# Kernel tuning notes

Hardware: AMD Instinct MI355X
Metric: run time of the kernel (lower is better)

Reference implementation:

```python
import jax, jax.numpy as jnp
import numpy as np

ALPHA = 0.2  # LeakyReLU negative slope
NEG_BIG = -9e15

def setup_inputs() -> dict:
    key = jax.random.key(0)
    k1, k2, k3, k4 = jax.random.split(key, 4)
    N, Fin, Fout = 8192, 256, 64
    h = jax.random.normal(k1, (N, Fin), dtype=jnp.float32)
    adj = jax.random.randint(k2, (N, N), 0, 2, dtype=jnp.int32)
    W = jax.random.normal(k3, (Fin, Fout), dtype=jnp.float32) * 0.1
    a = jax.random.normal(k4, (2 * Fout, 1), dtype=jnp.float32) * 0.1
    return {"h": h, "adj": adj, "W": W, "a": a}

def reference(h, adj, W, a):
    Fout = W.shape[1]
    Wh = h @ W                                # [N, Fout]
    # e_ij = leakyrelu([Wh_i ; Wh_j] . a) = leakyrelu(Wh_i.a1 + Wh_j.a2)
    a1 = a[:Fout, 0]                          # [Fout]
    a2 = a[Fout:, 0]                          # [Fout]
    s1 = Wh @ a1                              # [N]
    s2 = Wh @ a2                              # [N]
    e = jax.nn.leaky_relu(s1[:, None] + s2[None, :], negative_slope=ALPHA)  # [N, N]
    attention = jnp.where(adj > 0, e, jnp.float32(NEG_BIG))
    attention = jax.nn.softmax(attention, axis=1)
    # dropout p=0.0 (eval) -> identity
    h_prime = attention @ Wh                  # [N, Fout]
    return jax.nn.elu(h_prime)                # concat=True
```

## Files before the change

kernel.cpp:

```cpp
#include <hip/hip_runtime.h>
#include <hip/hip_bf16.h>


typedef __attribute__((ext_vector_type(8))) short bf16x8;
typedef __attribute__((ext_vector_type(16))) float f32x16;

#define LOG2E 1.4426950408889634f

__device__ __forceinline__ uint pk2o(float a, float b) {
    __hip_bfloat162 h = __float22bfloat162_rn(make_float2(a, b));
    union { __hip_bfloat162 b; uint u; } c; c.b = h; return c.u;
}
__device__ __forceinline__ ushort f2bf(float x) {
    union { __hip_bfloat16 b; ushort u; } c;
    c.b = __float2bfloat16(x);
    return c.u;
}
__device__ __forceinline__ float bf2f(ushort u) {
    union { ushort u; __hip_bfloat16 b; } c;
    c.u = u;
    return __bfloat162float(c.b);
}

__global__ __launch_bounds__(256) void k1_wh(
    const float* __restrict__ h, const float* __restrict__ W,
    const float* __restrict__ a,
    float* __restrict__ s1, float* __restrict__ Fg, float* __restrict__ Gg,
    ushort* __restrict__ pw_hi, ushort* __restrict__ pw_lo)
{
    __shared__ ushort whh[16][64], whl[16][64];
    const int l = threadIdx.x & 63;
    const int w = threadIdx.x >> 6;
    const int b = blockIdx.x;
    const int row0 = b * 16 + w * 4;

    float acc[4] = {0.f, 0.f, 0.f, 0.f};
    for (int k = 0; k < 256; k += 4) {
        float w0 = W[(k + 0) * 64 + l];
        float w1 = W[(k + 1) * 64 + l];
        float w2 = W[(k + 2) * 64 + l];
        float w3 = W[(k + 3) * 64 + l];
#pragma unroll
        for (int r = 0; r < 4; ++r) {
            const float4 hv = *reinterpret_cast<const float4*>(&h[(row0 + r) * 256 + k]);
            acc[r] = fmaf(hv.x, w0, acc[r]);
            acc[r] = fmaf(hv.y, w1, acc[r]);
            acc[r] = fmaf(hv.z, w2, acc[r]);
            acc[r] = fmaf(hv.w, w3, acc[r]);
        }
    }
    const float a1 = a[l];
    const float a2 = a[64 + l];
#pragma unroll
    for (int r = 0; r < 4; ++r) {
        const int row = row0 + r;
        float x1 = acc[r] * a1;
        float x2 = acc[r] * a2;
#pragma unroll
        for (int m = 32; m >= 1; m >>= 1) {
            x1 += __shfl_xor(x1, m);
            x2 += __shfl_xor(x2, m);
        }
        if (l == 0) {
            s1[row] = x1;
            Fg[row] = __builtin_amdgcn_exp2f(x2 * LOG2E);
            Gg[row] = __builtin_amdgcn_exp2f(0.2f * x2 * LOG2E);
        }
        const ushort hi = f2bf(acc[r]);
        const ushort lo = f2bf(acc[r] - bf2f(hi));
        whh[w * 4 + r][l] = hi;
        whl[w * 4 + r][l] = lo;
    }
    __syncthreads();
    const int ft = w & 1;
    const ushort (*src)[64] = (w < 2) ? whh : whl;
    ushort* dst = (w < 2) ? pw_hi : pw_lo;
    const int hh = l >> 5;
    union { bf16x8 v; ushort s[8]; } fr;
#pragma unroll
    for (int e = 0; e < 8; ++e)
        fr.s[e] = src[hh * 8 + e][ft * 32 + (l & 31)];
    *reinterpret_cast<bf16x8*>(&dst[(size_t)(b * 2 + ft) * 512 + l * 8]) = fr.v;
}


#define PGRP(G_, AV, RS) { \
    float p0_ = fmaxf(Ea[G_] * fv.x, Eb[G_] * gv.x); if ((AV).x <= 0) p0_ = 0.f; \
    float p1_ = fmaxf(Ea[G_] * fv.y, Eb[G_] * gv.y); if ((AV).y <= 0) p1_ = 0.f; \
    float p2_ = fmaxf(Ea[G_] * fv.z, Eb[G_] * gv.z); if ((AV).z <= 0) p2_ = 0.f; \
    float p3_ = fmaxf(Ea[G_] * fv.w, Eb[G_] * gv.w); if ((AV).w <= 0) p3_ = 0.f; \
    RS += (p0_ + p1_) + (p2_ + p3_); \
    *reinterpret_cast<uint2*>(&myp[(8 * (G_) + g8) * 38 + jc]) = \
        make_uint2(pk2o(p0_, p1_), pk2o(p2_, p3_)); \
}

__global__ __launch_bounds__(256, 4) void k2_attn(
    const int* __restrict__ adj,
    const float* __restrict__ s1g,
    const float* __restrict__ Fgl, const float* __restrict__ Ggl,
    const ushort* __restrict__ pw_hi, const ushort* __restrict__ pw_lo,
    float* __restrict__ pacc8, float* __restrict__ pden8)
{
    __shared__ __align__(16) unsigned char smem[18432];

    const int t   = threadIdx.x;
    const int l   = t & 63;
    const int wv  = t >> 6;
    const int qi  = blockIdx.x >> 3;
    const int jh  = blockIdx.x & 7;
    const int i0  = qi * 32;
    const int row = l & 31;
    const int kh  = l >> 5;
    const int g8  = l >> 3;
    const int jc  = (l & 7) * 4;

    float*  Fl  = reinterpret_cast<float*>(smem);
    float*  Gl  = reinterpret_cast<float*>(smem + 4096);
    ushort* myp = reinterpret_cast<ushort*>(smem + 8192) + wv * 1216;
    float (*dlds)[32] = reinterpret_cast<float(*)[32]>(smem + 17920);

    reinterpret_cast<float4*>(Fl)[t] =
        reinterpret_cast<const float4*>(Fgl + jh * 1024)[t];
    reinterpret_cast<float4*>(Gl)[t] =
        reinterpret_cast<const float4*>(Ggl + jh * 1024)[t];

    float Ea[4], Eb[4];
#pragma unroll
    for (int g = 0; g < 4; ++g) {
        const float s1v = s1g[i0 + 8 * g + g8];
        const float mq  = s1v + 16.0f;
        const float m   = fmaxf(mq, 0.2f * mq);
        Ea[g] = __builtin_amdgcn_exp2f((s1v - m) * LOG2E);
        Eb[g] = __builtin_amdgcn_exp2f(fmaf(0.2f, s1v, -m) * LOG2E);
    }
    __syncthreads();

    const int jb  = jh * 1024 + wv * 256;
    const int js0 = jb >> 4;
    const int* ap0 = adj + (size_t)(i0 + g8) * 8192 + jb + jc;
    const int* ap1 = ap0 + (size_t)8 * 8192;
    const int* ap2 = ap0 + (size_t)16 * 8192;
    const int* ap3 = ap0 + (size_t)24 * 8192;

    f32x16 acc0 = {0.f,0.f,0.f,0.f,0.f,0.f,0.f,0.f,0.f,0.f,0.f,0.f,0.f,0.f,0.f,0.f};
    f32x16 acc1 = {0.f,0.f,0.f,0.f,0.f,0.f,0.f,0.f,0.f,0.f,0.f,0.f,0.f,0.f,0.f,0.f};
    float rs0 = 0.f, rs1 = 0.f, rs2 = 0.f, rs3 = 0.f;

    int4 c0 = *reinterpret_cast<const int4*>(ap0);
    int4 c1 = *reinterpret_cast<const int4*>(ap1);
    int4 c2 = *reinterpret_cast<const int4*>(ap2);
    int4 c3 = *reinterpret_cast<const int4*>(ap3);

#pragma unroll
    for (int ms = 0; ms < 8; ++ms) {
        const int nm = (ms < 7) ? (ms + 1) * 32 : 7 * 32;
        const int4 n0 = *reinterpret_cast<const int4*>(ap0 + nm);
        const int4 n1 = *reinterpret_cast<const int4*>(ap1 + nm);
        const int4 n2 = *reinterpret_cast<const int4*>(ap2 + nm);
        const int4 n3 = *reinterpret_cast<const int4*>(ap3 + nm);
        const float4 fv = *reinterpret_cast<const float4*>(&Fl[wv * 256 + ms * 32 + jc]);
        const float4 gv = *reinterpret_cast<const float4*>(&Gl[wv * 256 + ms * 32 + jc]);

        PGRP(0, c0, rs0)
        PGRP(1, c1, rs1)
        PGRP(2, c2, rs2)
        PGRP(3, c3, rs3)

#pragma unroll
        for (int ksx = 0; ksx < 2; ++ksx) {
            const int js = js0 + ms * 2 + ksx;
            const bf16x8 ah0 = *reinterpret_cast<const bf16x8*>(&pw_hi[(size_t)(js * 2 + 0) * 512 + l * 8]);
            const bf16x8 al0 = *reinterpret_cast<const bf16x8*>(&pw_lo[(size_t)(js * 2 + 0) * 512 + l * 8]);
            const bf16x8 ah1 = *reinterpret_cast<const bf16x8*>(&pw_hi[(size_t)(js * 2 + 1) * 512 + l * 8]);
            const bf16x8 al1 = *reinterpret_cast<const bf16x8*>(&pw_lo[(size_t)(js * 2 + 1) * 512 + l * 8]);
            union { bf16x8 v; ushort4 q[2]; } bh;
            bh.q[0] = *reinterpret_cast<const ushort4*>(&myp[row * 38 + ksx * 16 + kh * 8]);
            bh.q[1] = *reinterpret_cast<const ushort4*>(&myp[row * 38 + ksx * 16 + kh * 8 + 4]);
            acc0 = __builtin_amdgcn_mfma_f32_32x32x16_bf16(ah0, bh.v, acc0, 0, 0, 0);
            acc0 = __builtin_amdgcn_mfma_f32_32x32x16_bf16(al0, bh.v, acc0, 0, 0, 0);
            acc1 = __builtin_amdgcn_mfma_f32_32x32x16_bf16(ah1, bh.v, acc1, 0, 0, 0);
            acc1 = __builtin_amdgcn_mfma_f32_32x32x16_bf16(al1, bh.v, acc1, 0, 0, 0);
        }
        c0 = n0; c1 = n1; c2 = n2; c3 = n3;
    }

#define RED8(RS) RS += __shfl_xor(RS, 1); RS += __shfl_xor(RS, 2); RS += __shfl_xor(RS, 4);
    RED8(rs0) RED8(rs1) RED8(rs2) RED8(rs3)
    if ((l & 7) == 0) {
        dlds[wv][g8]      = rs0;
        dlds[wv][8 + g8]  = rs1;
        dlds[wv][16 + g8] = rs2;
        dlds[wv][24 + g8] = rs3;
    }
    __syncthreads();

    if (wv == 0 && l < 32)
        pden8[(size_t)jh * 8192 + i0 + l] =
            dlds[0][l] + dlds[1][l] + dlds[2][l] + dlds[3][l];

    float* sldsc = reinterpret_cast<float*>(smem);
#pragma unroll
    for (int c = 0; c < 4; ++c) {
        if (wv != 0) {
            float4* d0 = reinterpret_cast<float4*>(&sldsc[(((wv - 1) * 2 + 0) * 64 + l) * 4]);
            float4* d1 = reinterpret_cast<float4*>(&sldsc[(((wv - 1) * 2 + 1) * 64 + l) * 4]);
            *d0 = make_float4(acc0[c*4+0], acc0[c*4+1], acc0[c*4+2], acc0[c*4+3]);
            *d1 = make_float4(acc1[c*4+0], acc1[c*4+1], acc1[c*4+2], acc1[c*4+3]);
        }
        __syncthreads();
        if (wv == 0) {
#pragma unroll
            for (int s = 0; s < 3; ++s) {
                const float4 v0 = *reinterpret_cast<const float4*>(&sldsc[((s * 2 + 0) * 64 + l) * 4]);
                const float4 v1 = *reinterpret_cast<const float4*>(&sldsc[((s * 2 + 1) * 64 + l) * 4]);
                acc0[c*4+0] += v0.x; acc0[c*4+1] += v0.y; acc0[c*4+2] += v0.z; acc0[c*4+3] += v0.w;
                acc1[c*4+0] += v1.x; acc1[c*4+1] += v1.y; acc1[c*4+2] += v1.z; acc1[c*4+3] += v1.w;
            }
        }
        __syncthreads();
    }

    if (wv == 0) {
        float* pb = pacc8 + ((size_t)jh * 8192 + i0 + row) * 64;
#pragma unroll
        for (int g = 0; g < 4; ++g) {
            *reinterpret_cast<float4*>(pb + 8 * g + 4 * kh) =
                make_float4(acc0[g*4+0], acc0[g*4+1], acc0[g*4+2], acc0[g*4+3]);
            *reinterpret_cast<float4*>(pb + 32 + 8 * g + 4 * kh) =
                make_float4(acc1[g*4+0], acc1[g*4+1], acc1[g*4+2], acc1[g*4+3]);
        }
    }
}

__global__ __launch_bounds__(256) void k3_fin(
    const float* __restrict__ pacc8, const float* __restrict__ pden8,
    float* __restrict__ out)
{
    const int idx = blockIdx.x * 256 + threadIdx.x;
    const int row = idx >> 4;
    float den = 0.f;
    float4 v = make_float4(0.f, 0.f, 0.f, 0.f);
#pragma unroll
    for (int p = 0; p < 8; ++p) {
        den += pden8[p * 8192 + row];
        const float4 u = reinterpret_cast<const float4*>(pacc8 + (size_t)p * 524288)[idx];
        v.x += u.x; v.y += u.y; v.z += u.z; v.w += u.w;
    }
    const float inv = 1.0f / den;
    float4 o; float x;
    x = v.x * inv; o.x = (x > 0.f) ? x : expm1f(x);
    x = v.y * inv; o.y = (x > 0.f) ? x : expm1f(x);
    x = v.z * inv; o.z = (x > 0.f) ? x : expm1f(x);
    x = v.w * inv; o.w = (x > 0.f) ? x : expm1f(x);
    reinterpret_cast<float4*>(out)[idx] = o;
}

extern "C" void kernel_launch(void* const* d_in, const int* in_sizes, int n_in,
                              void* d_out, int out_size, void* d_ws, size_t ws_size,
                              hipStream_t stream) {
    const float* h   = (const float*)d_in[0];
    const int*   adj = (const int*)d_in[1];
    const float* W   = (const float*)d_in[2];
    const float* a   = (const float*)d_in[3];
    float* out = (float*)d_out;

    float*  s1    = (float*)d_ws;
    float*  Fg    = s1 + 8192;
    float*  Gg    = Fg + 8192;
    ushort* pw_hi = (ushort*)(Gg + 8192);
    ushort* pw_lo = pw_hi + 512 * 1024;
    float*  pacc8 = (float*)(pw_lo + 512 * 1024);
    float*  pden8 = pacc8 + 8 * 8192 * 64;

    hipLaunchKernelGGL(k1_wh, dim3(512), dim3(256), 0, stream,
                       h, W, a, s1, Fg, Gg, pw_hi, pw_lo);
    hipLaunchKernelGGL(k2_attn, dim3(2048), dim3(256), 0, stream,
                       adj, s1, Fg, Gg, pw_hi, pw_lo, pacc8, pden8);
    hipLaunchKernelGGL(k3_fin, dim3(512), dim3(256), 0, stream,
                       pacc8, pden8, out);
}
```

Before: 102.3 us.

## Pre-pack adjacency into bitmasks in first kernel, consume bitmasks in attention kernel

The first kernel gains 2048 extra blocks that read the int32 adjacency matrix and use wave ballots to pack it into 64-bit masks laid out per attention block. The attention kernel then loads a 4KB mask tile into shared memory and tests bits, instead of streaming int32 adjacency values from global memory inside the main loop. The full adjacency read still happens once, now in the first kernel. This adds a mask write/read round trip and more shared memory per block, which could lower occupancy.

```diff
diff --git a/kernel.cpp b/kernel.cpp
--- a/kernel.cpp
+++ b/kernel.cpp
@@ -22,15 +22,43 @@
     return __bfloat162float(c.b);
 }
 
-__global__ __launch_bounds__(256) void k1_wh(
+__global__ __launch_bounds__(256) void k1c(
     const float* __restrict__ h, const float* __restrict__ W,
-    const float* __restrict__ a,
+    const float* __restrict__ a, const int* __restrict__ adj,
     float* __restrict__ s1, float* __restrict__ Fg, float* __restrict__ Gg,
-    ushort* __restrict__ pw_hi, ushort* __restrict__ pw_lo)
+    ushort* __restrict__ pw_hi, ushort* __restrict__ pw_lo,
+    unsigned long long* __restrict__ maskT)
 {
     __shared__ ushort whh[16][64], whl[16][64];
     const int l = threadIdx.x & 63;
     const int w = threadIdx.x >> 6;
+
+    if (blockIdx.x >= 512) {
+        const int cb = blockIdx.x - 512;
+        const int qi = cb >> 3;
+        const int jh = cb & 7;
+        const int i0 = qi * 32;
+        const uint4* ap = reinterpret_cast<const uint4*>(
+            adj + (size_t)i0 * 8192 + jh * 1024 + w * 256) + l;
+        unsigned long long* mout = maskT + (size_t)cb * 512 + w * 128;
+#pragma unroll 4
+        for (int r = 0; r < 32; ++r) {
+            const uint4 v = ap[(size_t)r * 2048];
+            const unsigned long long b0 = __ballot((int)v.x > 0);
+            const unsigned long long b1 = __ballot((int)v.y > 0);
+            const unsigned long long b2 = __ballot((int)v.z > 0);
+            const unsigned long long b3 = __ballot((int)v.w > 0);
+            if (l < 4) {
+                unsigned long long bb = b0;
+                if (l == 1) bb = b1;
+                if (l == 2) bb = b2;
+                if (l == 3) bb = b3;
+                mout[r * 4 + l] = bb;
+            }
+        }
+        return;
+    }
+
     const int b = blockIdx.x;
     const int row0 = b * 16 + w * 4;
 
@@ -84,87 +112,80 @@
 }
 
 
-#define PGRP(G_, AV, RS) { \
-    float p0_ = fmaxf(Ea[G_] * fv.x, Eb[G_] * gv.x); if ((AV).x <= 0) p0_ = 0.f; \
-    float p1_ = fmaxf(Ea[G_] * fv.y, Eb[G_] * gv.y); if ((AV).y <= 0) p1_ = 0.f; \
-    float p2_ = fmaxf(Ea[G_] * fv.z, Eb[G_] * gv.z); if ((AV).z <= 0) p2_ = 0.f; \
-    float p3_ = fmaxf(Ea[G_] * fv.w, Eb[G_] * gv.w); if ((AV).w <= 0) p3_ = 0.f; \
+#define PGRP(G_, RS) { \
+    const unsigned long long* qr_ = &mq[(w4 * 32 + 8 * (G_) + g8) * 4]; \
+    const unsigned long long q0_ = qr_[0], q1_ = qr_[1], q2_ = qr_[2], q3_ = qr_[3]; \
+    float p0_ = fmaxf(Ea[G_] * fv.x, Eb[G_] * gv.x); if (!((q0_ >> sh) & 1)) p0_ = 0.f; \
+    float p1_ = fmaxf(Ea[G_] * fv.y, Eb[G_] * gv.y); if (!((q1_ >> sh) & 1)) p1_ = 0.f; \
+    float p2_ = fmaxf(Ea[G_] * fv.z, Eb[G_] * gv.z); if (!((q2_ >> sh) & 1)) p2_ = 0.f; \
+    float p3_ = fmaxf(Ea[G_] * fv.w, Eb[G_] * gv.w); if (!((q3_ >> sh) & 1)) p3_ = 0.f; \
     RS += (p0_ + p1_) + (p2_ + p3_); \
     *reinterpret_cast<uint2*>(&myp[(8 * (G_) + g8) * 38 + jc]) = \
         make_uint2(pk2o(p0_, p1_), pk2o(p2_, p3_)); \
 }
 
 __global__ __launch_bounds__(256, 4) void k2_attn(
-    const int* __restrict__ adj,
+    const unsigned long long* __restrict__ maskT,
     const float* __restrict__ s1g,
     const float* __restrict__ Fgl, const float* __restrict__ Ggl,
     const ushort* __restrict__ pw_hi, const ushort* __restrict__ pw_lo,
     float* __restrict__ pacc8, float* __restrict__ pden8)
 {
-    __shared__ __align__(16) unsigned char smem[18432];
+    __shared__ __align__(16) unsigned char smem[22528];
 
     const int t   = threadIdx.x;
     const int l   = t & 63;
-    const int wv  = t >> 6;
+    const int w4  = t >> 6;
     const int qi  = blockIdx.x >> 3;
     const int jh  = blockIdx.x & 7;
     const int i0  = qi * 32;
     const int row = l & 31;
     const int kh  = l >> 5;
     const int g8  = l >> 3;
-    const int jc  = (l & 7) * 4;
+    const int lm  = l & 7;
+    const int jc  = lm * 4;
 
     float*  Fl  = reinterpret_cast<float*>(smem);
     float*  Gl  = reinterpret_cast<float*>(smem + 4096);
-    ushort* myp = reinterpret_cast<ushort*>(smem + 8192) + wv * 1216;
-    float (*dlds)[32] = reinterpret_cast<float(*)[32]>(smem + 17920);
+    unsigned long long* mq = reinterpret_cast<unsigned long long*>(smem + 8192);
+    ushort* myp = reinterpret_cast<ushort*>(smem + 12288) + w4 * 1216;
+    float (*dlds)[32] = reinterpret_cast<float(*)[32]>(smem + 22016);
 
     reinterpret_cast<float4*>(Fl)[t] =
         reinterpret_cast<const float4*>(Fgl + jh * 1024)[t];
     reinterpret_cast<float4*>(Gl)[t] =
         reinterpret_cast<const float4*>(Ggl + jh * 1024)[t];
+    reinterpret_cast<ulonglong2*>(mq)[t] =
+        reinterpret_cast<const ulonglong2*>(maskT + (size_t)blockIdx.x * 512)[t];
 
     float Ea[4], Eb[4];
 #pragma unroll
     for (int g = 0; g < 4; ++g) {
         const float s1v = s1g[i0 + 8 * g + g8];
-        const float mq  = s1v + 16.0f;
-        const float m   = fmaxf(mq, 0.2f * mq);
+        const float mq_ = s1v + 16.0f;
+        const float m   = fmaxf(mq_, 0.2f * mq_);
         Ea[g] = __builtin_amdgcn_exp2f((s1v - m) * LOG2E);
         Eb[g] = __builtin_amdgcn_exp2f(fmaf(0.2f, s1v, -m) * LOG2E);
     }
     __syncthreads();
 
-    const int jb  = jh * 1024 + wv * 256;
+    const int jb  = jh * 1024 + w4 * 256;
     const int js0 = jb >> 4;
-    const int* ap0 = adj + (size_t)(i0 + g8) * 8192 + jb + jc;
-    const int* ap1 = ap0 + (size_t)8 * 8192;
-    const int* ap2 = ap0 + (size_t)16 * 8192;
-    const int* ap3 = ap0 + (size_t)24 * 8192;
 
     f32x16 acc0 = {0.f,0.f,0.f,0.f,0.f,0.f,0.f,0.f,0.f,0.f,0.f,0.f,0.f,0.f,0.f,0.f};
     f32x16 acc1 = {0.f,0.f,0.f,0.f,0.f,0.f,0.f,0.f,0.f,0.f,0.f,0.f,0.f,0.f,0.f,0.f};
     float rs0 = 0.f, rs1 = 0.f, rs2 = 0.f, rs3 = 0.f;
 
-    int4 c0 = *reinterpret_cast<const int4*>(ap0);
-    int4 c1 = *reinterpret_cast<const int4*>(ap1);
-    int4 c2 = *reinterpret_cast<const int4*>(ap2);
-    int4 c3 = *reinterpret_cast<const int4*>(ap3);
-
 #pragma unroll
     for (int ms = 0; ms < 8; ++ms) {
-        const int nm = (ms < 7) ? (ms + 1) * 32 : 7 * 32;
-        const int4 n0 = *reinterpret_cast<const int4*>(ap0 + nm);
-        const int4 n1 = *reinterpret_cast<const int4*>(ap1 + nm);
-        const int4 n2 = *reinterpret_cast<const int4*>(ap2 + nm);
-        const int4 n3 = *reinterpret_cast<const int4*>(ap3 + nm);
-        const float4 fv = *reinterpret_cast<const float4*>(&Fl[wv * 256 + ms * 32 + jc]);
-        const float4 gv = *reinterpret_cast<const float4*>(&Gl[wv * 256 + ms * 32 + jc]);
-
-        PGRP(0, c0, rs0)
-        PGRP(1, c1, rs1)
-        PGRP(2, c2, rs2)
-        PGRP(3, c3, rs3)
+        const uint sh = ms * 8 + lm;
+        const float4 fv = *reinterpret_cast<const float4*>(&Fl[w4 * 256 + ms * 32 + jc]);
+        const float4 gv = *reinterpret_cast<const float4*>(&Gl[w4 * 256 + ms * 32 + jc]);
+
+        PGRP(0, rs0)
+        PGRP(1, rs1)
+        PGRP(2, rs2)
+        PGRP(3, rs3)
 
 #pragma unroll
         for (int ksx = 0; ksx < 2; ++ksx) {
@@ -181,34 +202,33 @@
             acc1 = __builtin_amdgcn_mfma_f32_32x32x16_bf16(ah1, bh.v, acc1, 0, 0, 0);
             acc1 = __builtin_amdgcn_mfma_f32_32x32x16_bf16(al1, bh.v, acc1, 0, 0, 0);
         }
-        c0 = n0; c1 = n1; c2 = n2; c3 = n3;
     }
 
 #define RED8(RS) RS += __shfl_xor(RS, 1); RS += __shfl_xor(RS, 2); RS += __shfl_xor(RS, 4);
     RED8(rs0) RED8(rs1) RED8(rs2) RED8(rs3)
-    if ((l & 7) == 0) {
-        dlds[wv][g8]      = rs0;
-        dlds[wv][8 + g8]  = rs1;
-        dlds[wv][16 + g8] = rs2;
-        dlds[wv][24 + g8] = rs3;
+    if (lm == 0) {
+        dlds[w4][g8]      = rs0;
+        dlds[w4][8 + g8]  = rs1;
+        dlds[w4][16 + g8] = rs2;
+        dlds[w4][24 + g8] = rs3;
     }
     __syncthreads();
 
-    if (wv == 0 && l < 32)
+    if (w4 == 0 && l < 32)
         pden8[(size_t)jh * 8192 + i0 + l] =
             dlds[0][l] + dlds[1][l] + dlds[2][l] + dlds[3][l];
 
     float* sldsc = reinterpret_cast<float*>(smem);
 #pragma unroll
     for (int c = 0; c < 4; ++c) {
-        if (wv != 0) {
-            float4* d0 = reinterpret_cast<float4*>(&sldsc[(((wv - 1) * 2 + 0) * 64 + l) * 4]);
-            float4* d1 = reinterpret_cast<float4*>(&sldsc[(((wv - 1) * 2 + 1) * 64 + l) * 4]);
+        if (w4 != 0) {
+            float4* d0 = reinterpret_cast<float4*>(&sldsc[(((w4 - 1) * 2 + 0) * 64 + l) * 4]);
+            float4* d1 = reinterpret_cast<float4*>(&sldsc[(((w4 - 1) * 2 + 1) * 64 + l) * 4]);
             *d0 = make_float4(acc0[c*4+0], acc0[c*4+1], acc0[c*4+2], acc0[c*4+3]);
             *d1 = make_float4(acc1[c*4+0], acc1[c*4+1], acc1[c*4+2], acc1[c*4+3]);
         }
         __syncthreads();
-        if (wv == 0) {
+        if (w4 == 0) {
 #pragma unroll
             for (int s = 0; s < 3; ++s) {
                 const float4 v0 = *reinterpret_cast<const float4*>(&sldsc[((s * 2 + 0) * 64 + l) * 4]);
@@ -220,7 +240,7 @@
         __syncthreads();
     }
 
-    if (wv == 0) {
+    if (w4 == 0) {
         float* pb = pacc8 + ((size_t)jh * 8192 + i0 + row) * 64;
 #pragma unroll
         for (int g = 0; g < 4; ++g) {
@@ -269,13 +289,15 @@
     float*  Gg    = Fg + 8192;
     ushort* pw_hi = (ushort*)(Gg + 8192);
     ushort* pw_lo = pw_hi + 512 * 1024;
-    float*  pacc8 = (float*)(pw_lo + 512 * 1024);
+    unsigned long long* maskT =
+        (unsigned long long*)(pw_lo + 512 * 1024);
+    float*  pacc8 = (float*)(maskT + 2048 * 512);
     float*  pden8 = pacc8 + 8 * 8192 * 64;
 
-    hipLaunchKernelGGL(k1_wh, dim3(512), dim3(256), 0, stream,
-                       h, W, a, s1, Fg, Gg, pw_hi, pw_lo);
+    hipLaunchKernelGGL(k1c, dim3(2560), dim3(256), 0, stream,
+                       h, W, a, adj, s1, Fg, Gg, pw_hi, pw_lo, maskT);
     hipLaunchKernelGGL(k2_attn, dim3(2048), dim3(256), 0, stream,
-                       adj, s1, Fg, Gg, pw_hi, pw_lo, pacc8, pden8);
+                       maskT, s1, Fg, Gg, pw_hi, pw_lo, pacc8, pden8);
     hipLaunchKernelGGL(k3_fin, dim3(512), dim3(256), 0, stream,
                        pacc8, pden8, out);
 }
```

New measurement: 158.6 us. 55.1% more time.
